# Kernel tuning notes

Measured on AMD Instinct MI355X. Metric: run time of the kernel, lower is better.

Reference implementation:

```python
import jax, jax.numpy as jnp
import numpy as np

B, S, L = 128, 512, 20  # batch, max seq length, g.max_word_length
VOCAB = 10000


def setup_inputs() -> dict:
    key = jax.random.key(0)
    k1, k2, k3 = jax.random.split(key, 3)
    lost_unit_id_seqs = jax.random.randint(k1, (B, S), 0, VOCAB, dtype=jnp.int32)
    # lengths in [L, S] so every batch element has viable spans
    lost_lengths = jax.random.randint(k2, (B,), L, S + 1, dtype=jnp.int32)
    p_weights = jax.random.uniform(k3, (B, S, L), dtype=jnp.float32)
    return {
        "lost_unit_id_seqs": lost_unit_id_seqs,
        "lost_lengths": lost_lengths,
        "p_weights": p_weights,
        "max_word_length": L,
    }


def reference(lost_unit_id_seqs, lost_lengths, p_weights, max_word_length):
    b, s = lost_unit_id_seqs.shape
    l = max_word_length
    n = b * s * l  # static upper bound on number of viable spans

    # _propose_candidates: enumerate all (start, span_length) pairs
    starts = jnp.arange(s, dtype=jnp.int32)[None, :, None]          # [1,S,1]
    lens = jnp.arange(1, l + 1, dtype=jnp.int32)[None, None, :]      # [1,1,L]
    ends = starts + lens - 1                                          # [1,S,L]

    viable = ends < lost_lengths[:, None, None]                       # [B,S,L] bool
    shape = viable.shape
    start_candidates = jnp.broadcast_to(starts, shape)
    end_candidates = jnp.broadcast_to(ends, shape)
    len_candidates = jnp.broadcast_to(lens, shape)
    batch_indices = jnp.broadcast_to(
        jnp.arange(b, dtype=jnp.int32)[:, None, None], shape)

    # boolean-mask stream compaction with static size (viable entries first,
    # tail padded with index 0; true count = viable.sum())
    flat_viable = viable.reshape(-1)
    idx = jnp.nonzero(flat_viable, size=n, fill_value=0)[0]           # [N]

    viable_starts = start_candidates.reshape(-1)[idx]
    viable_ends = end_candidates.reshape(-1)[idx]
    viable_lengths = len_candidates.reshape(-1)[idx]
    viable_batch_indices = batch_indices.reshape(-1)[idx]
    viable_p_weights = p_weights.reshape(-1)[idx]

    # 2D advanced-index gather of unit ids for each viable span
    max_length = jnp.max(lost_lengths)
    word_pos = jnp.minimum(
        viable_starts[:, None] + jnp.arange(l, dtype=jnp.int32)[None, :],
        max_length - 1)                                               # [N,L]
    viable_unit_id_seqs = lost_unit_id_seqs[viable_batch_indices[:, None], word_pos]

    return (viable, viable_batch_indices, viable_starts, viable_ends,
            viable_lengths, viable_unit_id_seqs, viable_p_weights,
            start_candidates, end_candidates, len_candidates)
```

## Files before the change

kernel.cpp:

```cpp
#include <hip/hip_runtime.h>
#include <stdint.h>

#define TPB 256
#define BB  128
#define SS  512
#define LLW 20
#define NN  (BB * SS * LLW)

static __device__ __forceinline__ void preamble(const int* __restrict__ lens,
                                                int* shC, int* shM, int* shLen,
                                                int t) {
  int len0 = (t < BB) ? lens[t] : 0;
  shLen[t] = len0;
  shC[t] = (t < BB) ? (LLW * len0 - (LLW * (LLW - 1)) / 2) : 0;
  shM[t] = len0;
  for (int off = 1; off < TPB; off <<= 1) {
    __syncthreads();
    int aC = shC[t]; int bC = (t >= off) ? shC[t - off] : 0;
    int aM = shM[t]; int bM = shM[t ^ off];
    __syncthreads();
    shC[t] = aC + bC;
    shM[t] = (aM > bM) ? aM : bM;
  }
  __syncthreads();
}

static __device__ __forceinline__ void invert(int k, const int* shC,
                                              const int* shLen, int K,
                                              int* pb, int* ps, int* pj) {
  int b = 0, s = 0, j = 0;
  if (k < K) {
    int lo = 0, hi = BB - 1;
    while (lo < hi) {
      int mid = (lo + hi) >> 1;
      if (shC[mid] > k) hi = mid; else lo = mid + 1;
    }
    b = lo;
    int base = (b == 0) ? 0 : shC[b - 1];
    int m    = k - base;
    int lenb = shLen[b];
    int full = LLW * (lenb - LLW + 1);
    if (m < full) {
      s = m / LLW;
      j = m - s * LLW;
    } else {
      int Cb = shC[b] - base;
      int tt = Cb - m;
      float rf = (sqrtf(8.0f * (float)tt + 1.0f) - 1.0f) * 0.5f;
      int r = (int)(rf + 0.5f);
      if (r * (r + 1) / 2 < tt) r++;
      if (r > 1 && r * (r - 1) / 2 >= tt) r--;
      s = lenb - r;
      j = r * (r + 1) / 2 - tt;
    }
  }
  *pb = b; *ps = s; *pj = j;
}

__global__ __launch_bounds__(TPB) void span_full(
    const int* __restrict__ seqs,
    const int* __restrict__ lens,
    const float* __restrict__ pw,
    float* __restrict__ out) {
  __shared__ int shC[TPB], shM[TPB], shLen[TPB];
  __shared__ int sBS[TPB];
  const int t = threadIdx.x;
  preamble(lens, shC, shM, shLen, t);
  const int K  = shC[BB - 1];
  const int ml = shM[0];

  const int gid = blockIdx.x * TPB + t;
  const size_t Nz = (size_t)NN;

  {
    int f   = gid;
    int row = f / LLW;
    int jj  = f - row * LLW;
    int b2  = row >> 9;
    int s2  = row & (SS - 1);
    int e2  = s2 + jj;
    out[f]           = (e2 < shLen[b2]) ? 1.0f : 0.0f;
    out[26 * Nz + f] = (float)s2;
    out[27 * Nz + f] = (float)e2;
    out[28 * Nz + f] = (float)(jj + 1);
  }
  {
    int k = gid, b, s, j;
    invert(k, shC, shLen, K, &b, &s, &j);
    out[Nz      + k] = (float)b;
    out[2 * Nz  + k] = (float)s;
    out[3 * Nz  + k] = (float)(s + j);
    out[4 * Nz  + k] = (float)(j + 1);
    out[25 * Nz + k] = pw[((size_t)b * SS + s) * LLW + j];
    sBS[t] = (b << 16) | s;
  }
  __syncthreads();
  {
    int ml1 = ml - 1;
    float4* udst = (float4*)(out + 5 * Nz + (size_t)blockIdx.x * (TPB * LLW));
#pragma unroll
    for (int c = 0; c < LLW / 4; c++) {
      int chunk = t + c * TPB;
      int krow  = chunk / 5;
      int e0    = (chunk - krow * 5) * 4;
      int bs    = sBS[krow];
      const int* srow = seqs + ((size_t)(bs >> 16) << 9);
      int s = bs & 0xFFFF;
      int p0 = s + e0;     if (p0 > ml1) p0 = ml1;
      int p1 = s + e0 + 1; if (p1 > ml1) p1 = ml1;
      int p2 = s + e0 + 2; if (p2 > ml1) p2 = ml1;
      int p3 = s + e0 + 3; if (p3 > ml1) p3 = ml1;
      float4 v;
      v.x = (float)srow[p0];
      v.y = (float)srow[p1];
      v.z = (float)srow[p2];
      v.w = (float)srow[p3];
      udst[chunk] = v;
    }
  }
}

extern "C" void kernel_launch(void* const* d_in, const int* in_sizes, int n_in,
                              void* d_out, int out_size, void* d_ws, size_t ws_size,
                              hipStream_t stream) {
  const int*   seqs = (const int*)d_in[0];
  const int*   lens = (const int*)d_in[1];
  const float* pw   = (const float*)d_in[2];
  float* out = (float*)d_out;

  span_full<<<NN / TPB, TPB, 0, stream>>>(seqs, lens, pw, out);
}
```

Measured before the change: 165.9 us.

## Process four spans per thread, vectorize stores, stage sequence rows in LDS

Each thread now handles four consecutive output elements, so grids shrink fourfold. The binary-search inversion runs once per thread and the remaining spans are found by incremental stepping. All per-element outputs are written as float4 stores. The block's batch rows of unit ids are copied into shared memory so the gather reads LDS instead of scattered global loads, with a global fallback when rows exceed the cap. The cost is more shared memory per block and fewer blocks to hide latency.

```diff
diff --git a/kernel.cpp b/kernel.cpp
--- a/kernel.cpp
+++ b/kernel.cpp
@@ -6,6 +6,10 @@
 #define SS  512
 #define LLW 20
 #define NN  (BB * SS * LLW)
+#define KPT 4
+#define KPB (TPB * KPT)
+#define MAXROWS 8
+#define RSTRIDE 516
 
 static __device__ __forceinline__ void preamble(const int* __restrict__ lens,
                                                 int* shC, int* shM, int* shLen,
@@ -25,17 +29,21 @@
   __syncthreads();
 }
 
+static __device__ __forceinline__ int batch_of(int k, const int* shC) {
+  int lo = 0, hi = BB - 1;
+  while (lo < hi) {
+    int mid = (lo + hi) >> 1;
+    if (shC[mid] > k) hi = mid; else lo = mid + 1;
+  }
+  return lo;
+}
+
 static __device__ __forceinline__ void invert(int k, const int* shC,
                                               const int* shLen, int K,
                                               int* pb, int* ps, int* pj) {
   int b = 0, s = 0, j = 0;
   if (k < K) {
-    int lo = 0, hi = BB - 1;
-    while (lo < hi) {
-      int mid = (lo + hi) >> 1;
-      if (shC[mid] > k) hi = mid; else lo = mid + 1;
-    }
-    b = lo;
+    b = batch_of(k, shC);
     int base = (b == 0) ? 0 : shC[b - 1];
     int m    = k - base;
     int lenb = shLen[b];
@@ -63,58 +71,101 @@
     const float* __restrict__ pw,
     float* __restrict__ out) {
   __shared__ int shC[TPB], shM[TPB], shLen[TPB];
-  __shared__ int sBS[TPB];
+  __shared__ int sBS[KPB];
+  __shared__ int sRows[MAXROWS * RSTRIDE];
   const int t = threadIdx.x;
   preamble(lens, shC, shM, shLen, t);
   const int K  = shC[BB - 1];
   const int ml = shM[0];
 
-  const int gid = blockIdx.x * TPB + t;
-  const size_t Nz = (size_t)NN;
+  const int gid    = blockIdx.x * TPB + t;
+  const int k0     = gid * KPT;
+  const int blk_k0 = blockIdx.x * KPB;
+  const size_t Nz  = (size_t)NN;
+
+  int kq0 = blk_k0;           if (kq0 > K - 1) kq0 = K - 1;
+  int kq1 = blk_k0 + KPB - 1; if (kq1 > K - 1) kq1 = K - 1;
+  const int bf = batch_of(kq0, shC);
+  int nrows = (blk_k0 < K) ? (batch_of(kq1, shC) - bf + 1) : 0;
+  if (nrows > MAXROWS) nrows = MAXROWS;
+  {
+    const int4* src = (const int4*)(seqs + (size_t)bf * SS);
+    for (int q = t; q < nrows * (SS / 4); q += TPB) {
+      int lin = q << 2;
+      int r = lin >> 9, p = lin & (SS - 1);
+      *(int4*)(sRows + r * RSTRIDE + p) = src[q];
+    }
+  }
 
   {
-    int f   = gid;
-    int row = f / LLW;
-    int jj  = f - row * LLW;
-    int b2  = row >> 9;
-    int s2  = row & (SS - 1);
-    int e2  = s2 + jj;
-    out[f]           = (e2 < shLen[b2]) ? 1.0f : 0.0f;
-    out[26 * Nz + f] = (float)s2;
-    out[27 * Nz + f] = (float)e2;
-    out[28 * Nz + f] = (float)(jj + 1);
+    float qv[KPT], qsc[KPT], qec[KPT], qlc[KPT];
+#pragma unroll
+    for (int i = 0; i < KPT; i++) {
+      int f   = k0 + i;
+      int row = f / LLW;
+      int jj  = f - row * LLW;
+      int b2  = row >> 9;
+      int s2  = row & (SS - 1);
+      int e2  = s2 + jj;
+      qv[i]  = (e2 < shLen[b2]) ? 1.0f : 0.0f;
+      qsc[i] = (float)s2; qec[i] = (float)e2; qlc[i] = (float)(jj + 1);
+    }
+    *(float4*)(out + k0)           = make_float4(qv[0], qv[1], qv[2], qv[3]);
+    *(float4*)(out + 26 * Nz + k0) = make_float4(qsc[0], qsc[1], qsc[2], qsc[3]);
+    *(float4*)(out + 27 * Nz + k0) = make_float4(qec[0], qec[1], qec[2], qec[3]);
+    *(float4*)(out + 28 * Nz + k0) = make_float4(qlc[0], qlc[1], qlc[2], qlc[3]);
   }
   {
-    int k = gid, b, s, j;
-    invert(k, shC, shLen, K, &b, &s, &j);
-    out[Nz      + k] = (float)b;
-    out[2 * Nz  + k] = (float)s;
-    out[3 * Nz  + k] = (float)(s + j);
-    out[4 * Nz  + k] = (float)(j + 1);
-    out[25 * Nz + k] = pw[((size_t)b * SS + s) * LLW + j];
-    sBS[t] = (b << 16) | s;
+    int b, s, j;
+    invert(k0, shC, shLen, K, &b, &s, &j);
+    float qb[KPT], qs[KPT], qe[KPT], ql[KPT], qp[KPT];
+#pragma unroll
+    for (int i = 0; i < KPT; i++) {
+      int ki = k0 + i;
+      int vb = 0, vs = 0, vj = 0;
+      if (ki < K) {
+        vb = b; vs = s; vj = j;
+        j++;
+        int lenb = shLen[b];
+        int cs = lenb - s; if (cs > LLW) cs = LLW;
+        if (j >= cs) { j = 0; s++; if (s >= lenb) { s = 0; b++; } }
+      }
+      qb[i] = (float)vb; qs[i] = (float)vs;
+      qe[i] = (float)(vs + vj); ql[i] = (float)(vj + 1);
+      qp[i] = pw[((size_t)vb * SS + vs) * LLW + vj];
+      sBS[t * KPT + i] = (vb << 16) | vs;
+    }
+    *(float4*)(out + Nz + k0)      = make_float4(qb[0], qb[1], qb[2], qb[3]);
+    *(float4*)(out + 2 * Nz + k0)  = make_float4(qs[0], qs[1], qs[2], qs[3]);
+    *(float4*)(out + 3 * Nz + k0)  = make_float4(qe[0], qe[1], qe[2], qe[3]);
+    *(float4*)(out + 4 * Nz + k0)  = make_float4(ql[0], ql[1], ql[2], ql[3]);
+    *(float4*)(out + 25 * Nz + k0) = make_float4(qp[0], qp[1], qp[2], qp[3]);
   }
   __syncthreads();
   {
     int ml1 = ml - 1;
-    float4* udst = (float4*)(out + 5 * Nz + (size_t)blockIdx.x * (TPB * LLW));
-#pragma unroll
-    for (int c = 0; c < LLW / 4; c++) {
+    float4* udst = (float4*)(out + 5 * Nz + (size_t)blk_k0 * LLW);
+    for (int c = 0; c < (KPB * (LLW / 4)) / TPB; c++) {
       int chunk = t + c * TPB;
       int krow  = chunk / 5;
-      int e0    = (chunk - krow * 5) * 4;
+      int e0    = (chunk - krow * 5) << 2;
       int bs    = sBS[krow];
-      const int* srow = seqs + ((size_t)(bs >> 16) << 9);
-      int s = bs & 0xFFFF;
+      int b = bs >> 16, s = bs & 0xFFFF;
       int p0 = s + e0;     if (p0 > ml1) p0 = ml1;
       int p1 = s + e0 + 1; if (p1 > ml1) p1 = ml1;
       int p2 = s + e0 + 2; if (p2 > ml1) p2 = ml1;
       int p3 = s + e0 + 3; if (p3 > ml1) p3 = ml1;
       float4 v;
-      v.x = (float)srow[p0];
-      v.y = (float)srow[p1];
-      v.z = (float)srow[p2];
-      v.w = (float)srow[p3];
+      int ridx = b - bf;
+      if ((unsigned)ridx < (unsigned)nrows) {
+        const int* rp = sRows + ridx * RSTRIDE;
+        v.x = (float)rp[p0]; v.y = (float)rp[p1];
+        v.z = (float)rp[p2]; v.w = (float)rp[p3];
+      } else {
+        const int* rp = seqs + (size_t)b * SS;
+        v.x = (float)rp[p0]; v.y = (float)rp[p1];
+        v.z = (float)rp[p2]; v.w = (float)rp[p3];
+      }
       udst[chunk] = v;
     }
   }
@@ -128,5 +179,5 @@
   const float* pw   = (const float*)d_in[2];
   float* out = (float*)d_out;
 
-  span_full<<<NN / TPB, TPB, 0, stream>>>(seqs, lens, pw, out);
+  span_full<<<NN / KPB, TPB, 0, stream>>>(seqs, lens, pw, out);
 }
```

New measurement: 161.9 us, median of 2. -2.4%, faster.
